# Optimization experiments

Hardware: AMD Instinct MI355X
Metric: run time of the kernel (lower is better)

The kernel has to match this reference:

```python
import jax, jax.numpy as jnp
import numpy as np

B, S, D_IN, D_MODEL = 4, 2048, 1024, 1024


def setup_inputs() -> dict:
    key = jax.random.key(0)
    ks = jax.random.split(key, 8)
    glorot = np.sqrt(6.0 / (D_IN + D_MODEL))
    inp = {
        "q": jax.random.normal(ks[0], (B, S, D_IN), dtype=jnp.float32),
        "k": jax.random.normal(ks[1], (B, S, D_IN), dtype=jnp.float32),
        "v": jax.random.normal(ks[2], (B, S, D_IN), dtype=jnp.float32),
        "mask": jnp.zeros((1, S, S), dtype=jnp.float32),
        # conv kernels with shape (1, look_back=1, d_in, d_model)
        "kernel_q": jax.random.uniform(ks[3], (1, 1, D_IN, D_MODEL), jnp.float32, -glorot, glorot),
        "kernel_k": jax.random.uniform(ks[4], (1, 1, D_IN, D_MODEL), jnp.float32, -glorot, glorot),
        "kernel_v": jax.random.uniform(ks[5], (1, 1, D_IN, D_MODEL), jnp.float32, -glorot, glorot),
        "bias_q": 0.05 * jax.random.normal(ks[6], (D_MODEL,), dtype=jnp.float32),
        "bias_k": 0.05 * jax.random.normal(ks[7], (D_MODEL,), dtype=jnp.float32),
        "bias_v": 0.05 * jax.random.normal(jax.random.fold_in(key, 7), (D_MODEL,), dtype=jnp.float32),
    }
    return inp


def reference(q, k, v, mask, kernel_q, kernel_k, kernel_v, bias_q, bias_k, bias_v):
    # look_back == 1: the (1,1,d_in,d_model) conv is a per-token linear projection.
    Wq, Wk, Wv = kernel_q[0, 0], kernel_k[0, 0], kernel_v[0, 0]  # [d_in, d_model]
    qp = jax.nn.relu(jnp.einsum("bsd,de->bse", q, Wq) + bias_q)  # [B,S,D]
    kp = jax.nn.relu(jnp.einsum("bsd,de->bse", k, Wk) + bias_k)
    vp = jax.nn.relu(jnp.einsum("bsd,de->bse", v, Wv) + bias_v)
    # unnormalized relu-attention: relu(QK^T)/sqrt(dk) + mask (no softmax)
    scores = jax.nn.relu(jnp.einsum("bqe,bke->bqk", qp, kp))  # [B,S,S]
    dk = jnp.asarray(kp.shape[-1], dtype=scores.dtype)
    logits = scores / jnp.sqrt(dk) + mask
    out = jax.nn.relu(jnp.einsum("bqk,bke->bqe", logits, vp))  # [B,S,D]
    return out
```

## Files before the change

### kernel.cpp

```cpp
#include <hip/hip_runtime.h>


#define B_ 4
#define S_ 2048
#define D_ 1024

typedef __attribute__((ext_vector_type(8))) short short8;
typedef __attribute__((ext_vector_type(4))) float f32x4;
typedef const __attribute__((address_space(1))) void* gas1;
typedef __attribute__((address_space(3))) void* las3;

static __device__ __forceinline__ short f2bf(float x) {
    union { float f; unsigned u; } un; un.f = x;
    unsigned r = un.u + 0x7fff + ((un.u >> 16) & 1);
    return (short)(r >> 16);
}

__global__ void cvt3_kernel(const float* __restrict__ q, const float* __restrict__ k,
                            const float* __restrict__ v, short* __restrict__ out) {
    const float* in = (blockIdx.y == 0) ? q : ((blockIdx.y == 1) ? k : v);
    size_t i = ((size_t)blockIdx.x * blockDim.x + threadIdx.x) * 8;
    short* o = out + (size_t)blockIdx.y * ((size_t)B_ * S_ * D_);
    float4 a = *(const float4*)(in + i);
    float4 b = *(const float4*)(in + i + 4);
    short8 r;
    r[0] = f2bf(a.x); r[1] = f2bf(a.y); r[2] = f2bf(a.z); r[3] = f2bf(a.w);
    r[4] = f2bf(b.x); r[5] = f2bf(b.y); r[6] = f2bf(b.z); r[7] = f2bf(b.w);
    *(short8*)(o + i) = r;
}

__global__ void make_wT_kernel(const float* __restrict__ Wq, const float* __restrict__ Wk,
                               const float* __restrict__ Wv, short* __restrict__ wT) {
    const float* W = (blockIdx.z == 0) ? Wq : ((blockIdx.z == 1) ? Wk : Wv);
    short* o = wT + (size_t)blockIdx.z * D_ * D_;
    __shared__ float t[32][33];
    int bx = blockIdx.x, by = blockIdx.y;
    int tx = threadIdx.x & 31, ty = threadIdx.x >> 5;
    #pragma unroll
    for (int r = ty; r < 32; r += 8)
        t[r][tx] = W[(size_t)(by * 32 + r) * D_ + bx * 32 + tx];
    __syncthreads();
    #pragma unroll
    for (int r = ty; r < 32; r += 8)
        o[(size_t)(bx * 32 + r) * D_ + by * 32 + tx] = f2bf(t[tx][r]);
}

__global__ void transpose_bf16_kernel(const short* __restrict__ in, short* __restrict__ out) {
    __shared__ short t[64][65];
    int b = blockIdx.z;
    int e0 = blockIdx.x * 64, s0 = blockIdx.y * 64;
    const short* src = in + (size_t)b * S_ * D_;
    short* dst = out + (size_t)b * D_ * S_;
    int tx = threadIdx.x & 63, ty = threadIdx.x >> 6;
    #pragma unroll
    for (int r = ty; r < 64; r += 4)
        t[r][tx] = src[(size_t)(s0 + r) * D_ + e0 + tx];
    __syncthreads();
    #pragma unroll
    for (int r = ty; r < 64; r += 4)
        dst[(size_t)(e0 + r) * S_ + s0 + tx] = t[tx][r];
}

template <int EPI>
__global__ __launch_bounds__(512, 2)
void gemm3b_kernel(const short* __restrict__ A, const short* __restrict__ B, void* __restrict__ Cv,
                   int K, int lda, int ldb, int ldc,
                   size_t sA, size_t sB, size_t sC,
                   const float* __restrict__ bias0, const float* __restrict__ bias1,
                   const float* __restrict__ bias2,
                   const float* __restrict__ mask, int ldmask) {
    constexpr int BM = 256, BN = 128;
    constexpr int ASZ = BM * 32;
    constexpr int BSZ = BN * 32;

    __shared__ short As[3][ASZ];
    __shared__ short Bs[3][BSZ];

    const int gx = gridDim.x, gy = gridDim.y;
    const int nwg = gx * gy * gridDim.z;
    const int flat = blockIdx.x + gx * (blockIdx.y + gy * blockIdx.z);
    const int swz = (flat & 7) * (nwg >> 3) + (flat >> 3);
    const int bx = swz % gx;
    const int rem = swz / gx;
    const int by = rem % gy;
    const int bz = rem / gy;

    const int m0 = bx * BM, n0 = by * BN;
    const short* Ab = A + (size_t)bz * sA;
    const short* Bb = B + (size_t)bz * sB;

    const int tid = threadIdx.x;
    const int lane = tid & 63;
    const int w = tid >> 6;
    const int wr = w >> 1, wc = w & 1;
    const int lr16 = lane & 15, kq = lane >> 4;
    const int NT = K >> 5;

    const int csrc = (((tid & 3) ^ ((tid >> 3) & 3)) << 3);

    auto stageA = [&](int buf, int kt) {
        if (kt >= NT) return;
        #pragma unroll
        for (int R = 0; R < 2; ++R) {
            int row = R * 128 + (tid >> 2);
            const short* src = Ab + (size_t)(m0 + row) * lda + kt * 32 + csrc;
            __builtin_amdgcn_global_load_lds((gas1)src, (las3)&As[buf][R * 4096 + tid * 8], 16, 0, 0);
        }
    };
    auto stageB = [&](int buf, int kt) {
        if (kt >= NT) return;
        int row = tid >> 2;
        const short* src = Bb + (size_t)(n0 + row) * ldb + kt * 32 + csrc;
        __builtin_amdgcn_global_load_lds((gas1)src, (las3)&Bs[buf][tid * 8], 16, 0, 0);
    };
    auto ldA = [&](int buf, int mi) -> short8 {
        int row = wr * 64 + mi * 16 + lr16;
        int col = (kq ^ ((row >> 1) & 3)) << 3;
        return *(const short8*)&As[buf][row * 32 + col];
    };
    auto ldB = [&](int buf, int ni) -> short8 {
        int row = wc * 64 + ni * 16 + lr16;
        int col = (kq ^ ((row >> 1) & 3)) << 3;
        return *(const short8*)&Bs[buf][row * 32 + col];
    };

    f32x4 acc[4][4] = {};

    stageA(0, 0); stageB(0, 0);
    stageA(1, 1); stageB(1, 1);
    asm volatile("s_waitcnt vmcnt(3)" ::: "memory");
    __builtin_amdgcn_s_barrier();

    int r0 = 0, r1 = 1, r2 = 2;
    #pragma unroll 1
    for (int t = 0; t < NT; ++t) {
        short8 a0 = ldA(r0, 0), a1 = ldA(r0, 1);
        short8 b0 = ldB(r0, 0), b1 = ldB(r0, 1), b2 = ldB(r0, 2), b3 = ldB(r0, 3);
        stageA(r2, t + 2);
        asm volatile("s_waitcnt lgkmcnt(0)" ::: "memory");
        __builtin_amdgcn_s_setprio(1);
        acc[0][0] = __builtin_amdgcn_mfma_f32_16x16x32_bf16(a0, b0, acc[0][0], 0, 0, 0);
        acc[0][1] = __builtin_amdgcn_mfma_f32_16x16x32_bf16(a0, b1, acc[0][1], 0, 0, 0);
        acc[0][2] = __builtin_amdgcn_mfma_f32_16x16x32_bf16(a0, b2, acc[0][2], 0, 0, 0);
        acc[0][3] = __builtin_amdgcn_mfma_f32_16x16x32_bf16(a0, b3, acc[0][3], 0, 0, 0);
        acc[1][0] = __builtin_amdgcn_mfma_f32_16x16x32_bf16(a1, b0, acc[1][0], 0, 0, 0);
        acc[1][1] = __builtin_amdgcn_mfma_f32_16x16x32_bf16(a1, b1, acc[1][1], 0, 0, 0);
        acc[1][2] = __builtin_amdgcn_mfma_f32_16x16x32_bf16(a1, b2, acc[1][2], 0, 0, 0);
        acc[1][3] = __builtin_amdgcn_mfma_f32_16x16x32_bf16(a1, b3, acc[1][3], 0, 0, 0);
        __builtin_amdgcn_s_setprio(0);
        __builtin_amdgcn_s_barrier();

        short8 a2 = ldA(r0, 2), a3 = ldA(r0, 3);
        stageB(r2, t + 2);
        asm volatile("s_waitcnt lgkmcnt(0)" ::: "memory");
        __builtin_amdgcn_s_setprio(1);
        acc[2][0] = __builtin_amdgcn_mfma_f32_16x16x32_bf16(a2, b0, acc[2][0], 0, 0, 0);
        acc[2][1] = __builtin_amdgcn_mfma_f32_16x16x32_bf16(a2, b1, acc[2][1], 0, 0, 0);
        acc[2][2] = __builtin_amdgcn_mfma_f32_16x16x32_bf16(a2, b2, acc[2][2], 0, 0, 0);
        acc[2][3] = __builtin_amdgcn_mfma_f32_16x16x32_bf16(a2, b3, acc[2][3], 0, 0, 0);
        acc[3][0] = __builtin_amdgcn_mfma_f32_16x16x32_bf16(a3, b0, acc[3][0], 0, 0, 0);
        acc[3][1] = __builtin_amdgcn_mfma_f32_16x16x32_bf16(a3, b1, acc[3][1], 0, 0, 0);
        acc[3][2] = __builtin_amdgcn_mfma_f32_16x16x32_bf16(a3, b2, acc[3][2], 0, 0, 0);
        acc[3][3] = __builtin_amdgcn_mfma_f32_16x16x32_bf16(a3, b3, acc[3][3], 0, 0, 0);
        __builtin_amdgcn_s_setprio(0);
        asm volatile("s_waitcnt vmcnt(3)" ::: "memory");
        __builtin_amdgcn_s_barrier();

        int tmp = r0; r0 = r1; r1 = r2; r2 = tmp;
    }

    short* Cs = (short*)Cv + (size_t)bz * sC;
    float* Cf = (float*)Cv + (size_t)bz * sC;
    const float* bias = (EPI == 0) ? ((bz == 0) ? bias0 : ((bz == 1) ? bias1 : bias2)) : nullptr;
    #pragma unroll
    for (int mi = 0; mi < 4; ++mi) {
        #pragma unroll
        for (int ni = 0; ni < 4; ++ni) {
            int n = n0 + wc * 64 + ni * 16 + lr16;
            int mb = m0 + wr * 64 + mi * 16 + kq * 4;
            #pragma unroll
            for (int j = 0; j < 4; ++j) {
                int m = mb + j;
                float val = acc[mi][ni][j];
                if constexpr (EPI == 0) {
                    val = fmaxf(val + bias[n], 0.f);
                    Cs[(size_t)m * ldc + n] = f2bf(val);
                } else if constexpr (EPI == 1) {
                    val = fmaxf(val, 0.f) * 0.03125f + mask[(size_t)m * ldmask + n];
                    Cs[(size_t)m * ldc + n] = f2bf(val);
                } else {
                    Cf[(size_t)m * ldc + n] = fmaxf(val, 0.f);
                }
            }
        }
    }
}

extern "C" void kernel_launch(void* const* d_in, const int* in_sizes, int n_in,
                              void* d_out, int out_size, void* d_ws, size_t ws_size,
                              hipStream_t stream) {
    const float* q    = (const float*)d_in[0];
    const float* k    = (const float*)d_in[1];
    const float* v    = (const float*)d_in[2];
    const float* mask = (const float*)d_in[3];
    const float* Wq   = (const float*)d_in[4];
    const float* Wk   = (const float*)d_in[5];
    const float* Wv   = (const float*)d_in[6];
    const float* bq   = (const float*)d_in[7];
    const float* bk   = (const float*)d_in[8];
    const float* bv   = (const float*)d_in[9];
    float* out = (float*)d_out;

    char* ws = (char*)d_ws;
    short* wT     = (short*)(ws);
    short* qkv_bf = (short*)(ws + 6291456);
    short* logits = (short*)(ws + 6291456);
    short* qkvp   = (short*)(ws + 56623104);
    short* qp     = qkvp;
    short* kp     = qkvp + (size_t)B_ * S_ * D_;
    short* vp     = qkvp + 2 * (size_t)B_ * S_ * D_;
    short* vpT    = qp;

    const size_t tok = (size_t)B_ * S_;
    const size_t tokD = tok * D_;

    make_wT_kernel<<<dim3(32, 32, 3), 256, 0, stream>>>(Wq, Wk, Wv, wT);

    cvt3_kernel<<<dim3(tokD / 8 / 256, 3), 256, 0, stream>>>(q, k, v, qkv_bf);

    gemm3b_kernel<0><<<dim3(32, 8, 3), 512, 0, stream>>>(
        qkv_bf, wT, qkvp, D_, D_, D_, D_,
        tokD, (size_t)D_ * D_, tokD, bq, bk, bv, nullptr, 0);

    gemm3b_kernel<1><<<dim3(8, 16, 4), 512, 0, stream>>>(
        qp, kp, logits, D_, D_, D_, S_,
        (size_t)S_ * D_, (size_t)S_ * D_, (size_t)S_ * S_,
        nullptr, nullptr, nullptr, mask, S_);

    transpose_bf16_kernel<<<dim3(D_ / 64, S_ / 64, B_), 256, 0, stream>>>(vp, vpT);

    gemm3b_kernel<2><<<dim3(8, 8, 4), 512, 0, stream>>>(
        logits, vpT, out, S_, S_, S_, D_,
        (size_t)S_ * S_, (size_t)D_ * S_, (size_t)S_ * D_,
        nullptr, nullptr, nullptr, nullptr, 0);
}
```

Before: 344.7 us.

## Fuse fp32-to-bf16 input conversion into projection GEMM and pre-convert mask to bf16

Removes the separate conversion kernel for q/k/v and adds a dedicated projection GEMM. It loads fp32 activations into registers, converts them to bf16 and writes them into swizzled LDS with a double-buffered pipeline, while the weights still arrive via global_load_lds. The mask is converted to bf16 once so the scores epilogue reads half the bytes. The block-index swizzle order is also changed to iterate N before M. The aim is to avoid writing and re-reading a 48MB bf16 copy of the inputs, at the cost of a more complex, register-heavy GEMM pipeline and a lossy bf16 mask.

Result: slower. 357.9 us (+3.8%).

```diff
diff --git a/kernel.cpp b/kernel.cpp
--- a/kernel.cpp
+++ b/kernel.cpp
@@ -6,6 +6,7 @@
 #define D_ 1024
 
 typedef __attribute__((ext_vector_type(8))) short short8;
+typedef __attribute__((ext_vector_type(4))) short short4v;
 typedef __attribute__((ext_vector_type(4))) float f32x4;
 typedef const __attribute__((address_space(1))) void* gas1;
 typedef __attribute__((address_space(3))) void* las3;
@@ -15,18 +16,9 @@
     unsigned r = un.u + 0x7fff + ((un.u >> 16) & 1);
     return (short)(r >> 16);
 }
-
-__global__ void cvt3_kernel(const float* __restrict__ q, const float* __restrict__ k,
-                            const float* __restrict__ v, short* __restrict__ out) {
-    const float* in = (blockIdx.y == 0) ? q : ((blockIdx.y == 1) ? k : v);
-    size_t i = ((size_t)blockIdx.x * blockDim.x + threadIdx.x) * 8;
-    short* o = out + (size_t)blockIdx.y * ((size_t)B_ * S_ * D_);
-    float4 a = *(const float4*)(in + i);
-    float4 b = *(const float4*)(in + i + 4);
-    short8 r;
-    r[0] = f2bf(a.x); r[1] = f2bf(a.y); r[2] = f2bf(a.z); r[3] = f2bf(a.w);
-    r[4] = f2bf(b.x); r[5] = f2bf(b.y); r[6] = f2bf(b.z); r[7] = f2bf(b.w);
-    *(short8*)(o + i) = r;
+static __device__ __forceinline__ float bf2f(short s) {
+    union { unsigned u; float f; } un; un.u = ((unsigned)(unsigned short)s) << 16;
+    return un.f;
 }
 
 __global__ void make_wT_kernel(const float* __restrict__ Wq, const float* __restrict__ Wk,
@@ -45,6 +37,16 @@
         o[(size_t)(bx * 32 + r) * D_ + by * 32 + tx] = f2bf(t[tx][r]);
 }
 
+__global__ void make_maskbf_kernel(const float* __restrict__ mask, short* __restrict__ mb) {
+    size_t i = ((size_t)blockIdx.x * blockDim.x + threadIdx.x) * 8;
+    float4 a = *(const float4*)(mask + i);
+    float4 b = *(const float4*)(mask + i + 4);
+    short8 r;
+    r[0] = f2bf(a.x); r[1] = f2bf(a.y); r[2] = f2bf(a.z); r[3] = f2bf(a.w);
+    r[4] = f2bf(b.x); r[5] = f2bf(b.y); r[6] = f2bf(b.z); r[7] = f2bf(b.w);
+    *(short8*)(mb + i) = r;
+}
+
 __global__ void transpose_bf16_kernel(const short* __restrict__ in, short* __restrict__ out) {
     __shared__ short t[64][65];
     int b = blockIdx.z;
@@ -61,29 +63,167 @@
         dst[(size_t)(e0 + r) * S_ + s0 + tx] = t[tx][r];
 }
 
+__global__ __launch_bounds__(512, 2)
+void projf_kernel(const float* __restrict__ q, const float* __restrict__ k,
+                  const float* __restrict__ v, const short* __restrict__ wT,
+                  short* __restrict__ outp,
+                  const float* __restrict__ bq, const float* __restrict__ bk,
+                  const float* __restrict__ bv) {
+    constexpr int NT = D_ / 32;
+    __shared__ short As[2][256 * 32];
+    __shared__ short Bs[2][128 * 32];
+
+    const int gx = 32, gy = 8;
+    const int nwg = 768;
+    const int flat = blockIdx.x + gx * (blockIdx.y + gy * blockIdx.z);
+    const int swz = (flat & 7) * (nwg >> 3) + (flat >> 3);
+    const int by = swz % gy;
+    const int rem = swz / gy;
+    const int bx = rem % gx;
+    const int bz = rem / gx;
+
+    const float* Af = (bz == 0) ? q : ((bz == 1) ? k : v);
+    const short* Bb = wT + (size_t)bz * D_ * D_;
+    const float* bias = (bz == 0) ? bq : ((bz == 1) ? bk : bv);
+    short* Cs = outp + (size_t)bz * ((size_t)B_ * S_ * D_);
+
+    const int m0 = bx * 256, n0 = by * 128;
+    const int tid = threadIdx.x;
+    const int lane = tid & 63;
+    const int w = tid >> 6;
+    const int wr = w >> 1, wc = w & 1;
+    const int lr16 = lane & 15, kq = lane >> 4;
+
+    const int csrcB = (((tid & 3) ^ ((tid >> 3) & 3)) << 3);
+    auto stageBgl = [&](int buf, int kt) {
+        int row = tid >> 2;
+        const short* src = Bb + (size_t)(n0 + row) * D_ + kt * 32 + csrcB;
+        __builtin_amdgcn_global_load_lds((gas1)src, (las3)&Bs[buf][tid * 8], 16, 0, 0);
+    };
+    auto ldgA = [&](float4* aw, int kt) {
+        #pragma unroll
+        for (int R = 0; R < 4; ++R) {
+            int row = R * 64 + (tid >> 3);
+            aw[R] = *(const float4*)(Af + (size_t)(m0 + row) * D_ + kt * 32 + (tid & 7) * 4);
+        }
+    };
+    auto dswriteA = [&](int buf, const float4* aw) {
+        #pragma unroll
+        for (int R = 0; R < 4; ++R) {
+            int row = R * 64 + (tid >> 3);
+            int c = tid & 7;
+            int slot = (c >> 1) ^ ((row >> 1) & 3);
+            short4v s;
+            s[0] = f2bf(aw[R].x); s[1] = f2bf(aw[R].y);
+            s[2] = f2bf(aw[R].z); s[3] = f2bf(aw[R].w);
+            *(short4v*)&As[buf][row * 32 + slot * 8 + (c & 1) * 4] = s;
+        }
+    };
+    auto ldA = [&](int buf, int mi) -> short8 {
+        int row = wr * 64 + mi * 16 + lr16;
+        int col = (kq ^ ((row >> 1) & 3)) << 3;
+        return *(const short8*)&As[buf][row * 32 + col];
+    };
+    auto ldB = [&](int buf, int ni) -> short8 {
+        int row = wc * 64 + ni * 16 + lr16;
+        int col = (kq ^ ((row >> 1) & 3)) << 3;
+        return *(const short8*)&Bs[buf][row * 32 + col];
+    };
+
+    f32x4 acc[4][4] = {};
+    float4 s0a[4], s1a[4];
+
+    stageBgl(0, 0);
+    __builtin_amdgcn_sched_barrier(0);
+    ldgA(s0a, 0);
+    __builtin_amdgcn_sched_barrier(0);
+    ldgA(s1a, 1);
+    asm volatile("s_waitcnt vmcnt(4)" ::: "memory");
+    dswriteA(0, s0a);
+    asm volatile("s_waitcnt lgkmcnt(0)" ::: "memory");
+    __builtin_amdgcn_s_barrier();
+
+    auto tileBody = [&](int t, float4* awWr, float4* awLd) {
+        const int p = t & 1;
+        short8 a0 = ldA(p, 0), a1 = ldA(p, 1);
+        short8 b0 = ldB(p, 0), b1 = ldB(p, 1), b2 = ldB(p, 2), b3 = ldB(p, 3);
+        if (t + 1 < NT) stageBgl(p ^ 1, t + 1);
+        __builtin_amdgcn_sched_barrier(0);
+        if (t + 2 < NT) ldgA(awLd, t + 2);
+        asm volatile("s_waitcnt lgkmcnt(0)" ::: "memory");
+        __builtin_amdgcn_s_setprio(1);
+        acc[0][0] = __builtin_amdgcn_mfma_f32_16x16x32_bf16(a0, b0, acc[0][0], 0, 0, 0);
+        acc[0][1] = __builtin_amdgcn_mfma_f32_16x16x32_bf16(a0, b1, acc[0][1], 0, 0, 0);
+        acc[0][2] = __builtin_amdgcn_mfma_f32_16x16x32_bf16(a0, b2, acc[0][2], 0, 0, 0);
+        acc[0][3] = __builtin_amdgcn_mfma_f32_16x16x32_bf16(a0, b3, acc[0][3], 0, 0, 0);
+        acc[1][0] = __builtin_amdgcn_mfma_f32_16x16x32_bf16(a1, b0, acc[1][0], 0, 0, 0);
+        acc[1][1] = __builtin_amdgcn_mfma_f32_16x16x32_bf16(a1, b1, acc[1][1], 0, 0, 0);
+        acc[1][2] = __builtin_amdgcn_mfma_f32_16x16x32_bf16(a1, b2, acc[1][2], 0, 0, 0);
+        acc[1][3] = __builtin_amdgcn_mfma_f32_16x16x32_bf16(a1, b3, acc[1][3], 0, 0, 0);
+        __builtin_amdgcn_s_setprio(0);
+        __builtin_amdgcn_s_barrier();
+        short8 a2 = ldA(p, 2), a3 = ldA(p, 3);
+        asm volatile("s_waitcnt lgkmcnt(0)" ::: "memory");
+        __builtin_amdgcn_s_setprio(1);
+        acc[2][0] = __builtin_amdgcn_mfma_f32_16x16x32_bf16(a2, b0, acc[2][0], 0, 0, 0);
+        acc[2][1] = __builtin_amdgcn_mfma_f32_16x16x32_bf16(a2, b1, acc[2][1], 0, 0, 0);
+        acc[2][2] = __builtin_amdgcn_mfma_f32_16x16x32_bf16(a2, b2, acc[2][2], 0, 0, 0);
+        acc[2][3] = __builtin_amdgcn_mfma_f32_16x16x32_bf16(a2, b3, acc[2][3], 0, 0, 0);
+        acc[3][0] = __builtin_amdgcn_mfma_f32_16x16x32_bf16(a3, b0, acc[3][0], 0, 0, 0);
+        acc[3][1] = __builtin_amdgcn_mfma_f32_16x16x32_bf16(a3, b1, acc[3][1], 0, 0, 0);
+        acc[3][2] = __builtin_amdgcn_mfma_f32_16x16x32_bf16(a3, b2, acc[3][2], 0, 0, 0);
+        acc[3][3] = __builtin_amdgcn_mfma_f32_16x16x32_bf16(a3, b3, acc[3][3], 0, 0, 0);
+        __builtin_amdgcn_s_setprio(0);
+        if (t < NT - 2)       asm volatile("s_waitcnt vmcnt(5)" ::: "memory");
+        else if (t == NT - 2) asm volatile("s_waitcnt vmcnt(1)" ::: "memory");
+        if (t + 1 < NT) {
+            dswriteA(p ^ 1, awWr);
+            asm volatile("s_waitcnt lgkmcnt(0)" ::: "memory");
+        }
+        if (t < NT - 2)       asm volatile("s_waitcnt vmcnt(4)" ::: "memory");
+        else if (t == NT - 2) asm volatile("s_waitcnt vmcnt(0)" ::: "memory");
+        __builtin_amdgcn_s_barrier();
+    };
+
+    #pragma unroll 1
+    for (int I = 0; I < NT / 2; ++I) {
+        tileBody(2 * I,     s1a, s0a);
+        tileBody(2 * I + 1, s0a, s1a);
+    }
+
+    #pragma unroll
+    for (int mi = 0; mi < 4; ++mi) {
+        #pragma unroll
+        for (int ni = 0; ni < 4; ++ni) {
+            int n = n0 + wc * 64 + ni * 16 + lr16;
+            int mb = m0 + wr * 64 + mi * 16 + kq * 4;
+            #pragma unroll
+            for (int j = 0; j < 4; ++j) {
+                float val = fmaxf(acc[mi][ni][j] + bias[n], 0.f);
+                Cs[(size_t)(mb + j) * D_ + n] = f2bf(val);
+            }
+        }
+    }
+}
+
 template <int EPI>
 __global__ __launch_bounds__(512, 2)
 void gemm3b_kernel(const short* __restrict__ A, const short* __restrict__ B, void* __restrict__ Cv,
                    int K, int lda, int ldb, int ldc,
                    size_t sA, size_t sB, size_t sC,
-                   const float* __restrict__ bias0, const float* __restrict__ bias1,
-                   const float* __restrict__ bias2,
-                   const float* __restrict__ mask, int ldmask) {
+                   const short* __restrict__ maskb, int ldmask) {
     constexpr int BM = 256, BN = 128;
-    constexpr int ASZ = BM * 32;
-    constexpr int BSZ = BN * 32;
-
-    __shared__ short As[3][ASZ];
-    __shared__ short Bs[3][BSZ];
+    __shared__ short As[3][BM * 32];
+    __shared__ short Bs[3][BN * 32];
 
     const int gx = gridDim.x, gy = gridDim.y;
     const int nwg = gx * gy * gridDim.z;
     const int flat = blockIdx.x + gx * (blockIdx.y + gy * blockIdx.z);
     const int swz = (flat & 7) * (nwg >> 3) + (flat >> 3);
-    const int bx = swz % gx;
-    const int rem = swz / gx;
-    const int by = rem % gy;
-    const int bz = rem / gy;
+    const int by = swz % gy;
+    const int rem = swz / gy;
+    const int bx = rem % gx;
+    const int bz = rem / gx;
 
     const int m0 = bx * BM, n0 = by * BN;
     const short* Ab = A + (size_t)bz * sA;
@@ -171,7 +311,6 @@
 
     short* Cs = (short*)Cv + (size_t)bz * sC;
     float* Cf = (float*)Cv + (size_t)bz * sC;
-    const float* bias = (EPI == 0) ? ((bz == 0) ? bias0 : ((bz == 1) ? bias1 : bias2)) : nullptr;
     #pragma unroll
     for (int mi = 0; mi < 4; ++mi) {
         #pragma unroll
@@ -182,11 +321,8 @@
             for (int j = 0; j < 4; ++j) {
                 int m = mb + j;
                 float val = acc[mi][ni][j];
-                if constexpr (EPI == 0) {
-                    val = fmaxf(val + bias[n], 0.f);
-                    Cs[(size_t)m * ldc + n] = f2bf(val);
-                } else if constexpr (EPI == 1) {
-                    val = fmaxf(val, 0.f) * 0.03125f + mask[(size_t)m * ldmask + n];
+                if constexpr (EPI == 1) {
+                    val = fmaxf(val, 0.f) * 0.03125f + bf2f(maskb[(size_t)m * ldmask + n]);
                     Cs[(size_t)m * ldc + n] = f2bf(val);
                 } else {
                     Cf[(size_t)m * ldc + n] = fmaxf(val, 0.f);
@@ -213,34 +349,28 @@
 
     char* ws = (char*)d_ws;
     short* wT     = (short*)(ws);
-    short* qkv_bf = (short*)(ws + 6291456);
-    short* logits = (short*)(ws + 6291456);
-    short* qkvp   = (short*)(ws + 56623104);
+    short* maskbf = (short*)(ws + 6291456);
+    short* qkvp   = (short*)(ws + 14680064);
     short* qp     = qkvp;
     short* kp     = qkvp + (size_t)B_ * S_ * D_;
     short* vp     = qkvp + 2 * (size_t)B_ * S_ * D_;
+    short* logits = (short*)(ws + 65011712);
     short* vpT    = qp;
 
-    const size_t tok = (size_t)B_ * S_;
-    const size_t tokD = tok * D_;
-
     make_wT_kernel<<<dim3(32, 32, 3), 256, 0, stream>>>(Wq, Wk, Wv, wT);
-
-    cvt3_kernel<<<dim3(tokD / 8 / 256, 3), 256, 0, stream>>>(q, k, v, qkv_bf);
-
-    gemm3b_kernel<0><<<dim3(32, 8, 3), 512, 0, stream>>>(
-        qkv_bf, wT, qkvp, D_, D_, D_, D_,
-        tokD, (size_t)D_ * D_, tokD, bq, bk, bv, nullptr, 0);
+    make_maskbf_kernel<<<(S_ * S_ / 8 / 256), 256, 0, stream>>>(mask, maskbf);
+
+    projf_kernel<<<dim3(32, 8, 3), 512, 0, stream>>>(q, k, v, wT, qkvp, bq, bk, bv);
 
     gemm3b_kernel<1><<<dim3(8, 16, 4), 512, 0, stream>>>(
         qp, kp, logits, D_, D_, D_, S_,
         (size_t)S_ * D_, (size_t)S_ * D_, (size_t)S_ * S_,
-        nullptr, nullptr, nullptr, mask, S_);
+        maskbf, S_);
 
     transpose_bf16_kernel<<<dim3(D_ / 64, S_ / 64, B_), 256, 0, stream>>>(vp, vpT);
 
     gemm3b_kernel<2><<<dim3(8, 8, 4), 512, 0, stream>>>(
         logits, vpT, out, S_, S_, S_, D_,
         (size_t)S_ * S_, (size_t)D_ * S_, (size_t)S_ * D_,
-        nullptr, nullptr, nullptr, nullptr, 0);
-}
+        nullptr, 0);
+}
```
